# Optimization experiments

Hardware: AMD Instinct MI355X
Metric: run time of the kernel (lower is better)

## Reference

```python
import jax, jax.numpy as jnp
import numpy as np

B, M, K = 32, 64, 36
DS, DX, DQ, H = 512, 128, 512, 256


def setup_inputs() -> dict:
    key = jax.random.key(0)
    ks = jax.random.split(key, 11)
    sc = lambda fan_in: 1.0 / np.sqrt(fan_in)
    return {
        "s2": jax.random.normal(ks[0], (B, M, DS), jnp.float32),
        "x0": jax.random.normal(ks[1], (B, K, DX), jnp.float32),
        "q": jax.random.normal(ks[2], (B, DQ), jnp.float32),
        # score MLP: Linear(DS+DX+DQ -> H), ReLU, Linear(H -> 1)
        "score_w1": jax.random.normal(ks[3], (DS + DX + DQ, H), jnp.float32) * sc(DS + DX + DQ),
        "score_b1": jax.random.normal(ks[4], (H,), jnp.float32) * 0.01,
        "score_w2": jax.random.normal(ks[5], (H, 1), jnp.float32) * sc(H),
        "score_b2": jax.random.normal(ks[6], (1,), jnp.float32) * 0.01,
        # h MLP: Linear(DS -> H), ReLU, Linear(H -> DX)
        "h_w1": jax.random.normal(ks[7], (DS, H), jnp.float32) * sc(DS),
        "h_b1": jax.random.normal(ks[8], (H,), jnp.float32) * 0.01,
        "h_w2": jax.random.normal(ks[9], (H, DX), jnp.float32) * sc(H),
        "h_b2": jax.random.normal(ks[10], (DX,), jnp.float32) * 0.01,
    }


def reference(s2, x0, q, score_w1, score_b1, score_w2, score_b2, h_w1, h_b1, h_w2, h_b2):
    ds = s2.shape[-1]
    dx = x0.shape[-1]
    # First score Linear over concat [s_exp, x_exp, q_exp] decomposes into
    # block matmuls (same math as Linear on the concat, no 4D concat tensor).
    w_s = score_w1[:ds]            # (DS, H)
    w_x = score_w1[ds:ds + dx]     # (DX, H)
    w_q = score_w1[ds + dx:]       # (DQ, H)
    pre_s = jnp.einsum('bmd,dh->bmh', s2, w_s)   # (b, m, H)
    pre_x = jnp.einsum('bkd,dh->bkh', x0, w_x)   # (b, k, H)
    pre_q = q @ w_q                              # (b, H)
    hidden = jax.nn.relu(pre_s[:, :, None, :] + pre_x[:, None, :, :]
                         + pre_q[:, None, None, :] + score_b1)  # (b, m, k, H)
    logits = jnp.einsum('bmkh,h->bmk', hidden, score_w2[:, 0]) + score_b2[0]
    att = jax.nn.softmax(logits, axis=1)         # softmax over m
    h_s = jax.nn.relu(s2 @ h_w1 + h_b1) @ h_w2 + h_b2  # (b, m, DX)
    agg = jnp.einsum('bmk,bmf->bkf', att, h_s)   # (b, k, DX)
    return jnp.concatenate([x0, agg], axis=-1)   # (b, k, 2*DX)
```

## Files before the change

kernel.cpp:

```cpp
#include <hip/hip_runtime.h>

#define B_  32
#define M_  64
#define K_  36
#define DS_ 512
#define DX_ 128
#define DQ_ 512
#define H_  256

#define S2B 1024
#define PXB 288
#define QPB 32

__global__ __launch_bounds__(512, 6) void kern1(
    const float* __restrict__ s2,
    const float* __restrict__ x0,
    const float* __restrict__ q,
    const float* __restrict__ score_w1,
    const float* __restrict__ score_b1,
    const float* __restrict__ h_w1,
    const float* __restrict__ h_b1,
    float* __restrict__ pre_s,
    float* __restrict__ h1r,
    float* __restrict__ px,
    float* __restrict__ qpre)
{
    __shared__ float comb[4 * H_];
    const int t   = threadIdx.x;
    const int bid = blockIdx.x;
    const int h   = t & 255;
    const int kh  = __builtin_amdgcn_readfirstlane(t >> 8);

    if (bid < S2B) {
        const int tile = bid >> 1, mat = bid & 1;
        const float* W  = mat ? h_w1 : score_w1;
        const float* A  = s2 + (size_t)tile * 4 * DS_ + kh * 256;
        const float* Wp = W + (size_t)(kh * 256) * H_ + h;

        float acc[4];
        #pragma unroll
        for (int r = 0; r < 4; ++r) acc[r] = 0.f;

        #pragma unroll 2
        for (int k = 0; k < 256; k += 4) {
            const float b0 = Wp[(size_t)(k + 0) * H_];
            const float b1 = Wp[(size_t)(k + 1) * H_];
            const float b2 = Wp[(size_t)(k + 2) * H_];
            const float b3 = Wp[(size_t)(k + 3) * H_];
            #pragma unroll
            for (int r = 0; r < 4; ++r) {
                const float4 a = *(const float4*)(A + (size_t)r * DS_ + k);
                acc[r] = fmaf(a.x, b0, acc[r]);
                acc[r] = fmaf(a.y, b1, acc[r]);
                acc[r] = fmaf(a.z, b2, acc[r]);
                acc[r] = fmaf(a.w, b3, acc[r]);
            }
        }
        if (kh) {
            #pragma unroll
            for (int r = 0; r < 4; ++r) comb[r * H_ + h] = acc[r];
        }
        __syncthreads();
        if (!kh) {
            if (!mat) {
                float* dst = pre_s + (size_t)tile * 4 * H_ + h;
                #pragma unroll
                for (int r = 0; r < 4; ++r)
                    dst[(size_t)r * H_] = acc[r] + comb[r * H_ + h];
            } else {
                const float b1v = h_b1[h];
                float* dst = h1r + (size_t)tile * 4 * H_ + h;
                #pragma unroll
                for (int r = 0; r < 4; ++r)
                    dst[(size_t)r * H_] =
                        fmaxf(acc[r] + comb[r * H_ + h] + b1v, 0.f);
            }
        }

    } else if (bid < S2B + PXB) {
        const int tile = bid - S2B;
        const float* A  = x0 + (size_t)tile * 4 * DX_ + kh * 64;
        const float* Wp = score_w1 + (size_t)(DS_ + kh * 64) * H_ + h;

        float acc[4];
        #pragma unroll
        for (int r = 0; r < 4; ++r) acc[r] = 0.f;

        #pragma unroll 2
        for (int k = 0; k < 64; k += 4) {
            const float b0 = Wp[(size_t)(k + 0) * H_];
            const float b1 = Wp[(size_t)(k + 1) * H_];
            const float b2 = Wp[(size_t)(k + 2) * H_];
            const float b3 = Wp[(size_t)(k + 3) * H_];
            #pragma unroll
            for (int r = 0; r < 4; ++r) {
                const float4 a = *(const float4*)(A + (size_t)r * DX_ + k);
                acc[r] = fmaf(a.x, b0, acc[r]);
                acc[r] = fmaf(a.y, b1, acc[r]);
                acc[r] = fmaf(a.z, b2, acc[r]);
                acc[r] = fmaf(a.w, b3, acc[r]);
            }
        }
        if (kh) {
            #pragma unroll
            for (int r = 0; r < 4; ++r) comb[r * H_ + h] = acc[r];
        }
        __syncthreads();
        if (!kh) {
            const float b1v = score_b1[h];
            float* dst = px + (size_t)tile * 4 * H_ + h;
            #pragma unroll
            for (int r = 0; r < 4; ++r)
                dst[(size_t)r * H_] = acc[r] + comb[r * H_ + h] + b1v;
        }

    } else {
        const int b = bid - (S2B + PXB);
        const float* qp = q + (size_t)b * DQ_ + kh * 256;
        const float* wq = score_w1 + (size_t)(DS_ + DX_ + kh * 256) * H_ + h;
        float a0 = 0.f, a1 = 0.f, a2 = 0.f, a3 = 0.f;
        #pragma unroll 2
        for (int d = 0; d < 256; d += 4) {
            const float4 q4 = *(const float4*)(qp + d);
            a0 = fmaf(q4.x, wq[(size_t)(d + 0) * H_], a0);
            a1 = fmaf(q4.y, wq[(size_t)(d + 1) * H_], a1);
            a2 = fmaf(q4.z, wq[(size_t)(d + 2) * H_], a2);
            a3 = fmaf(q4.w, wq[(size_t)(d + 3) * H_], a3);
        }
        const float s = (a0 + a1) + (a2 + a3);
        if (kh) comb[h] = s;
        __syncthreads();
        if (!kh) qpre[(size_t)b * H_ + h] = s + comb[h];
    }
}

__global__ __launch_bounds__(256) void kern2(
    const float* __restrict__ h1r,
    const float* __restrict__ h_w2,
    float* __restrict__ hs)
{
    __shared__ float A[8 * H_];
    const int t  = threadIdx.x;
    const int r0 = blockIdx.x * 8;

    #pragma unroll
    for (int i = 0; i < 2; ++i) {
        const int flat = t * 4 + i * 1024;
        *(float4*)&A[flat] = *(const float4*)(h1r + (size_t)r0 * H_ + flat);
    }
    __syncthreads();

    const int f  = t & 127;
    const int rg = t >> 7;
    const float* Ar  = &A[rg * 4 * H_];
    const float* w2p = h_w2 + f;

    float o0 = 0.f, o1 = 0.f, o2 = 0.f, o3 = 0.f;
    #pragma unroll 2
    for (int k = 0; k < H_; k += 4) {
        const float w0  = w2p[(size_t)(k + 0) * DX_];
        const float w1  = w2p[(size_t)(k + 1) * DX_];
        const float w2v = w2p[(size_t)(k + 2) * DX_];
        const float w3  = w2p[(size_t)(k + 3) * DX_];
        const float4 a0 = *(const float4*)&Ar[0 * H_ + k];
        const float4 a1 = *(const float4*)&Ar[1 * H_ + k];
        const float4 a2 = *(const float4*)&Ar[2 * H_ + k];
        const float4 a3 = *(const float4*)&Ar[3 * H_ + k];
        o0 = fmaf(a0.x, w0, o0); o0 = fmaf(a0.y, w1, o0);
        o0 = fmaf(a0.z, w2v, o0); o0 = fmaf(a0.w, w3, o0);
        o1 = fmaf(a1.x, w0, o1); o1 = fmaf(a1.y, w1, o1);
        o1 = fmaf(a1.z, w2v, o1); o1 = fmaf(a1.w, w3, o1);
        o2 = fmaf(a2.x, w0, o2); o2 = fmaf(a2.y, w1, o2);
        o2 = fmaf(a2.z, w2v, o2); o2 = fmaf(a2.w, w3, o2);
        o3 = fmaf(a3.x, w0, o3); o3 = fmaf(a3.y, w1, o3);
        o3 = fmaf(a3.z, w2v, o3); o3 = fmaf(a3.w, w3, o3);
    }
    float* dst = hs + ((size_t)r0 + rg * 4) * DX_ + f;
    dst[0 * DX_] = o0;
    dst[1 * DX_] = o1;
    dst[2 * DX_] = o2;
    dst[3 * DX_] = o3;
}

__global__ __launch_bounds__(256) void kern3(
    const float* __restrict__ pre_s,
    const float* __restrict__ px,
    const float* __restrict__ qpre,
    const float* __restrict__ score_w2,
    const float* __restrict__ hs,
    const float* __restrict__ h_b2,
    const float* __restrict__ x0,
    float* __restrict__ out)
{
    __shared__ float logit[M_];
    __shared__ float att[M_];
    __shared__ float pr[DX_];

    const int t    = threadIdx.x;
    const int bk   = blockIdx.x;
    const int b    = bk / K_;
    const int lane = t & 63, wave = t >> 6;
    const int hq   = lane << 2;

    float4 c4, v4;
    {
        const float4 qv = *(const float4*)(qpre + (size_t)b * H_ + hq);
        const float4 pv = *(const float4*)(px + (size_t)bk * H_ + hq);
        c4.x = qv.x + pv.x; c4.y = qv.y + pv.y;
        c4.z = qv.z + pv.z; c4.w = qv.w + pv.w;
        v4 = *(const float4*)(score_w2 + hq);
    }

    const float* ps = pre_s + (size_t)b * M_ * H_;
    #pragma unroll 2
    for (int mi = 0; mi < 16; ++mi) {
        const int m = wave * 16 + mi;
        const float4 p = *(const float4*)(ps + (size_t)m * H_ + hq);
        float x = fmaxf(p.x + c4.x, 0.f) * v4.x
                + fmaxf(p.y + c4.y, 0.f) * v4.y
                + fmaxf(p.z + c4.z, 0.f) * v4.z
                + fmaxf(p.w + c4.w, 0.f) * v4.w;
        #pragma unroll
        for (int off = 32; off > 0; off >>= 1)
            x += __shfl_xor(x, off, 64);
        if (lane == 0) logit[m] = x;
    }
    __syncthreads();

    if (wave == 0) {
        const float L = logit[lane];
        float mx = L;
        #pragma unroll
        for (int off = 32; off > 0; off >>= 1)
            mx = fmaxf(mx, __shfl_xor(mx, off, 64));
        const float e = expf(L - mx);
        float sm = e;
        #pragma unroll
        for (int off = 32; off > 0; off >>= 1)
            sm += __shfl_xor(sm, off, 64);
        att[lane] = e / sm;
    }
    __syncthreads();

    const int f = t & 127, mh = t >> 7;
    {
        const float* hsp = hs + ((size_t)b * M_ + mh * 32) * DX_ + f;
        float r = 0.f;
        #pragma unroll 4
        for (int m2 = 0; m2 < 32; ++m2)
            r = fmaf(att[mh * 32 + m2], hsp[(size_t)m2 * DX_], r);
        if (mh) pr[f] = r;
        __syncthreads();
        if (!mh)
            out[(size_t)bk * (2 * DX_) + DX_ + f] = r + pr[f] + h_b2[f];
    }
    if (t < DX_)
        out[(size_t)bk * (2 * DX_) + t] = x0[(size_t)bk * DX_ + t];
}

extern "C" void kernel_launch(void* const* d_in, const int* in_sizes, int n_in,
                              void* d_out, int out_size, void* d_ws, size_t ws_size,
                              hipStream_t stream) {
    (void)in_sizes; (void)n_in; (void)out_size; (void)ws_size;
    const float* s2       = (const float*)d_in[0];
    const float* x0       = (const float*)d_in[1];
    const float* q        = (const float*)d_in[2];
    const float* score_w1 = (const float*)d_in[3];
    const float* score_b1 = (const float*)d_in[4];
    const float* score_w2 = (const float*)d_in[5];
    const float* h_w1     = (const float*)d_in[7];
    const float* h_b1     = (const float*)d_in[8];
    const float* h_w2     = (const float*)d_in[9];
    const float* h_b2     = (const float*)d_in[10];
    float* out = (float*)d_out;

    float* ws    = (float*)d_ws;
    float* pre_s = ws;
    float* h1r   = pre_s + (size_t)B_ * M_ * H_;
    float* px    = h1r   + (size_t)B_ * M_ * H_;
    float* qpre  = px    + (size_t)B_ * K_ * H_;
    float* hs    = qpre  + (size_t)B_ * H_;

    kern1<<<S2B + PXB + QPB, 512, 0, stream>>>(
        s2, x0, q, score_w1, score_b1, h_w1, h_b1, pre_s, h1r, px, qpre);
    kern2<<<256, 256, 0, stream>>>(h1r, h_w2, hs);
    kern3<<<B_ * K_, 256, 0, stream>>>(pre_s, px, qpre, score_w2, hs, h_b2,
                                       x0, out);
}
```

Before: 128.5 us.

## Fuse second h-MLP layer into kern1 and stage activations in LDS

After: 131.1 us. 2.0% more time.

```diff
diff --git a/kernel.cpp b/kernel.cpp
--- a/kernel.cpp
+++ b/kernel.cpp
@@ -20,12 +20,16 @@
     const float* __restrict__ score_b1,
     const float* __restrict__ h_w1,
     const float* __restrict__ h_b1,
+    const float* __restrict__ h_w2,
     float* __restrict__ pre_s,
-    float* __restrict__ h1r,
     float* __restrict__ px,
-    float* __restrict__ qpre)
+    float* __restrict__ qpre,
+    float* __restrict__ hs)
 {
+    __shared__ float As[4 * DS_];
     __shared__ float comb[4 * H_];
+    __shared__ float hre[4 * H_];
+
     const int t   = threadIdx.x;
     const int bid = blockIdx.x;
     const int h   = t & 255;
@@ -33,9 +37,16 @@
 
     if (bid < S2B) {
         const int tile = bid >> 1, mat = bid & 1;
-        const float* W  = mat ? h_w1 : score_w1;
-        const float* A  = s2 + (size_t)tile * 4 * DS_ + kh * 256;
+        const float* W = mat ? h_w1 : score_w1;
+
+        {
+            const float* Asrc = s2 + (size_t)tile * 4 * DS_;
+            *(float4*)&As[t * 4] = *(const float4*)(Asrc + t * 4);
+        }
+        __syncthreads();
+
         const float* Wp = W + (size_t)(kh * 256) * H_ + h;
+        const int ab = kh * 256;
 
         float acc[4];
         #pragma unroll
@@ -49,38 +60,62 @@
             const float b3 = Wp[(size_t)(k + 3) * H_];
             #pragma unroll
             for (int r = 0; r < 4; ++r) {
-                const float4 a = *(const float4*)(A + (size_t)r * DS_ + k);
+                const float4 a = *(const float4*)&As[r * DS_ + ab + k];
                 acc[r] = fmaf(a.x, b0, acc[r]);
                 acc[r] = fmaf(a.y, b1, acc[r]);
                 acc[r] = fmaf(a.z, b2, acc[r]);
                 acc[r] = fmaf(a.w, b3, acc[r]);
             }
         }
+
         if (kh) {
             #pragma unroll
             for (int r = 0; r < 4; ++r) comb[r * H_ + h] = acc[r];
         }
         __syncthreads();
-        if (!kh) {
-            if (!mat) {
+
+        if (!mat) {
+            if (!kh) {
                 float* dst = pre_s + (size_t)tile * 4 * H_ + h;
                 #pragma unroll
                 for (int r = 0; r < 4; ++r)
                     dst[(size_t)r * H_] = acc[r] + comb[r * H_ + h];
-            } else {
+            }
+        } else {
+            if (!kh) {
                 const float b1v = h_b1[h];
-                float* dst = h1r + (size_t)tile * 4 * H_ + h;
                 #pragma unroll
                 for (int r = 0; r < 4; ++r)
-                    dst[(size_t)r * H_] =
+                    hre[r * H_ + h] =
                         fmaxf(acc[r] + comb[r * H_ + h] + b1v, 0.f);
             }
+            __syncthreads();
+
+            const int row = t >> 7;
+            const int f   = t & 127;
+            const float* w2p = h_w2 + f;
+            float o0 = 0.f, o1 = 0.f, o2 = 0.f, o3 = 0.f;
+            #pragma unroll 2
+            for (int k = 0; k < H_; k += 4) {
+                o0 = fmaf(hre[row * H_ + k + 0], w2p[(size_t)(k + 0) * DX_], o0);
+                o1 = fmaf(hre[row * H_ + k + 1], w2p[(size_t)(k + 1) * DX_], o1);
+                o2 = fmaf(hre[row * H_ + k + 2], w2p[(size_t)(k + 2) * DX_], o2);
+                o3 = fmaf(hre[row * H_ + k + 3], w2p[(size_t)(k + 3) * DX_], o3);
+            }
+            hs[((size_t)tile * 4 + row) * DX_ + f] = (o0 + o1) + (o2 + o3);
         }
 
     } else if (bid < S2B + PXB) {
         const int tile = bid - S2B;
-        const float* A  = x0 + (size_t)tile * 4 * DX_ + kh * 64;
+
+        if (t < 128) {
+            const float* Asrc = x0 + (size_t)tile * 4 * DX_;
+            *(float4*)&As[t * 4] = *(const float4*)(Asrc + t * 4);
+        }
+        __syncthreads();
+
         const float* Wp = score_w1 + (size_t)(DS_ + kh * 64) * H_ + h;
+        const int ab = kh * 64;
 
         float acc[4];
         #pragma unroll
@@ -94,7 +129,7 @@
             const float b3 = Wp[(size_t)(k + 3) * H_];
             #pragma unroll
             for (int r = 0; r < 4; ++r) {
-                const float4 a = *(const float4*)(A + (size_t)r * DX_ + k);
+                const float4 a = *(const float4*)&As[r * DX_ + ab + k];
                 acc[r] = fmaf(a.x, b0, acc[r]);
                 acc[r] = fmaf(a.y, b1, acc[r]);
                 acc[r] = fmaf(a.z, b2, acc[r]);
@@ -116,12 +151,19 @@
 
     } else {
         const int b = bid - (S2B + PXB);
-        const float* qp = q + (size_t)b * DQ_ + kh * 256;
+
+        if (t < 128) {
+            const float* Asrc = q + (size_t)b * DQ_;
+            *(float4*)&As[t * 4] = *(const float4*)(Asrc + t * 4);
+        }
+        __syncthreads();
+
         const float* wq = score_w1 + (size_t)(DS_ + DX_ + kh * 256) * H_ + h;
+        const int qb = kh * 256;
         float a0 = 0.f, a1 = 0.f, a2 = 0.f, a3 = 0.f;
         #pragma unroll 2
         for (int d = 0; d < 256; d += 4) {
-            const float4 q4 = *(const float4*)(qp + d);
+            const float4 q4 = *(const float4*)&As[qb + d];
             a0 = fmaf(q4.x, wq[(size_t)(d + 0) * H_], a0);
             a1 = fmaf(q4.y, wq[(size_t)(d + 1) * H_], a1);
             a2 = fmaf(q4.z, wq[(size_t)(d + 2) * H_], a2);
@@ -132,54 +174,6 @@
         __syncthreads();
         if (!kh) qpre[(size_t)b * H_ + h] = s + comb[h];
     }
-}
-
-__global__ __launch_bounds__(256) void kern2(
-    const float* __restrict__ h1r,
-    const float* __restrict__ h_w2,
-    float* __restrict__ hs)
-{
-    __shared__ float A[8 * H_];
-    const int t  = threadIdx.x;
-    const int r0 = blockIdx.x * 8;
-
-    #pragma unroll
-    for (int i = 0; i < 2; ++i) {
-        const int flat = t * 4 + i * 1024;
-        *(float4*)&A[flat] = *(const float4*)(h1r + (size_t)r0 * H_ + flat);
-    }
-    __syncthreads();
-
-    const int f  = t & 127;
-    const int rg = t >> 7;
-    const float* Ar  = &A[rg * 4 * H_];
-    const float* w2p = h_w2 + f;
-
-    float o0 = 0.f, o1 = 0.f, o2 = 0.f, o3 = 0.f;
-    #pragma unroll 2
-    for (int k = 0; k < H_; k += 4) {
-        const float w0  = w2p[(size_t)(k + 0) * DX_];
-        const float w1  = w2p[(size_t)(k + 1) * DX_];
-        const float w2v = w2p[(size_t)(k + 2) * DX_];
-        const float w3  = w2p[(size_t)(k + 3) * DX_];
-        const float4 a0 = *(const float4*)&Ar[0 * H_ + k];
-        const float4 a1 = *(const float4*)&Ar[1 * H_ + k];
-        const float4 a2 = *(const float4*)&Ar[2 * H_ + k];
-        const float4 a3 = *(const float4*)&Ar[3 * H_ + k];
-        o0 = fmaf(a0.x, w0, o0); o0 = fmaf(a0.y, w1, o0);
-        o0 = fmaf(a0.z, w2v, o0); o0 = fmaf(a0.w, w3, o0);
-        o1 = fmaf(a1.x, w0, o1); o1 = fmaf(a1.y, w1, o1);
-        o1 = fmaf(a1.z, w2v, o1); o1 = fmaf(a1.w, w3, o1);
-        o2 = fmaf(a2.x, w0, o2); o2 = fmaf(a2.y, w1, o2);
-        o2 = fmaf(a2.z, w2v, o2); o2 = fmaf(a2.w, w3, o2);
-        o3 = fmaf(a3.x, w0, o3); o3 = fmaf(a3.y, w1, o3);
-        o3 = fmaf(a3.z, w2v, o3); o3 = fmaf(a3.w, w3, o3);
-    }
-    float* dst = hs + ((size_t)r0 + rg * 4) * DX_ + f;
-    dst[0 * DX_] = o0;
-    dst[1 * DX_] = o1;
-    dst[2 * DX_] = o2;
-    dst[3 * DX_] = o3;
 }
 
 __global__ __launch_bounds__(256) void kern3(
@@ -276,14 +270,13 @@
 
     float* ws    = (float*)d_ws;
     float* pre_s = ws;
-    float* h1r   = pre_s + (size_t)B_ * M_ * H_;
-    float* px    = h1r   + (size_t)B_ * M_ * H_;
+    float* px    = pre_s + (size_t)B_ * M_ * H_;
     float* qpre  = px    + (size_t)B_ * K_ * H_;
     float* hs    = qpre  + (size_t)B_ * H_;
 
     kern1<<<S2B + PXB + QPB, 512, 0, stream>>>(
-        s2, x0, q, score_w1, score_b1, h_w1, h_b1, pre_s, h1r, px, qpre);
-    kern2<<<256, 256, 0, stream>>>(h1r, h_w2, hs);
+        s2, x0, q, score_w1, score_b1, h_w1, h_b1, h_w2,
+        pre_s, px, qpre, hs);
     kern3<<<B_ * K_, 256, 0, stream>>>(pre_s, px, qpre, score_w2, hs, h_b2,
                                        x0, out);
 }
```
